# Performance work log

Hardware: AMD Instinct MI355X
Metric: run time of the kernel (lower is better)

## Reference

```python
import jax, jax.numpy as jnp
import numpy as np

NUM_BREAKPOINTS = 100  # module default
IMG_SHAPE = (1, 1, 4096, 8192)  # B must be 1: PWL(num_channels=1) sees (C*H*W, B)


def setup_inputs() -> dict:
    key = jax.random.key(0)
    k1, k2, k3, k4 = jax.random.split(key, 4)
    x = jax.random.uniform(k1, IMG_SHAPE, dtype=jnp.float32)
    # torchpwl.PWL parameters (num_channels=1): breakpoint x-positions, per-segment
    # slopes, and bias (function value at the leftmost breakpoint).
    x_positions = jax.random.uniform(k2, (1, NUM_BREAKPOINTS), dtype=jnp.float32)
    slopes = 1.0 + 0.1 * jax.random.normal(k3, (1, NUM_BREAKPOINTS), dtype=jnp.float32)
    biases = 0.05 * jax.random.normal(k4, (1,), dtype=jnp.float32)
    return {"x": x, "x_positions": x_positions, "slopes": slopes, "biases": biases}


def _pwl(x_flat, x_positions, slopes, biases):
    # Sloped piecewise-linear function (torchpwl.BaseSlopedPWL math), 1 channel.
    # x_flat: (N,), x_positions/slopes: (1, K), biases: (1,)
    K = x_positions.shape[1]
    sorted_x = jnp.sort(x_positions, axis=1)                     # (1, K)
    skips = jnp.roll(sorted_x, -1, axis=1) - sorted_x            # last entry never used
    cumsums = jnp.cumsum(skips * slopes, axis=1)[:, :-1]         # (1, K-1)
    betas = jnp.concatenate([biases[:, None], biases[:, None] + cumsums], axis=1)  # (1, K)
    # segment index: (# breakpoints <= x) clamped to [1, K], minus 1
    idx = jnp.clip(jnp.searchsorted(sorted_x[0], x_flat, side="right"), 1, K) - 1
    return betas[0, idx] + (x_flat - sorted_x[0, idx]) * slopes[0, idx]


def reference(x, x_positions, slopes, biases):
    # forward: flatten -> PWL -> clip(0,1) -> reshape (original returns [out])
    y = _pwl(x.reshape(-1), x_positions, slopes, biases)
    return jnp.clip(y, 0.0, 1.0).reshape(x.shape)
```

## Files before the change

### kernel.cpp

```cpp
#include <hip/hip_runtime.h>

#define K   100
#define NB  1024
#define BS  512
#define NBLK 1024

typedef float fvec4 __attribute__((ext_vector_type(4)));

__device__ __forceinline__ float pwl_eval(float xv,
                                          const float2* __restrict__ s_bab,
                                          const float* __restrict__ s_x,
                                          const float2* __restrict__ s_ab) {
  int b = (int)(xv * (float)NB);
  b = min(max(b, 0), NB - 1);
  float2 ab = s_bab[b];
  if (__float_as_uint(ab.x) == 0x7f800000u) {
    unsigned p = __float_as_uint(ab.y);
    int lo = (int)(p & 0xffffu);
    int hi = (int)(p >> 16);
    while (lo < hi) {
      int mid = (lo + hi) >> 1;
      if (s_x[mid] <= xv) lo = mid + 1; else hi = mid;
    }
    int idx = min(max(lo, 1), K) - 1;
    ab = s_ab[idx];
  }
  float y = fmaf(xv, ab.x, ab.y);
  return fminf(fmaxf(y, 0.0f), 1.0f);
}

__global__ __launch_bounds__(BS) void pwl_fused_kernel(
    const fvec4* __restrict__ x, const float* __restrict__ xp,
    const float* __restrict__ sl, const float* __restrict__ bias,
    fvec4* __restrict__ out, int n4, int n) {
  __shared__ float s_pos[K];
  __shared__ float s_slope[K];
  __shared__ float s_x[K];
  __shared__ float s_c[K];
  __shared__ float2 s_ab[K];
  __shared__ unsigned short s_cnt[NB + 1];
  __shared__ float2 s_bab[NB];

  const int t = threadIdx.x;

  if (t < K) { s_pos[t] = xp[t]; s_slope[t] = sl[t]; }
  __syncthreads();

  if (t < K) {
    float v = s_pos[t];
    int r = 0;
    for (int j = 0; j < K; ++j) {
      float u = s_pos[j];
      r += ((u < v) || (u == v && j < t)) ? 1 : 0;
    }
    s_x[r] = v;
  }
  __syncthreads();

  if (t < K - 1) s_c[t] = (s_x[t + 1] - s_x[t]) * s_slope[t];
  __syncthreads();
  for (int off = 1; off < K - 1; off <<= 1) {
    float v = 0.0f;
    if (t >= off && t < K - 1) v = s_c[t - off];
    __syncthreads();
    if (t < K - 1) s_c[t] += v;
    __syncthreads();
  }
  if (t < K) {
    float beta = bias[0] + (t ? s_c[t - 1] : 0.0f);
    float a = s_slope[t];
    s_ab[t] = make_float2(a, beta - s_x[t] * a);
  }
  __syncthreads();

  for (int e = t; e <= NB; e += BS) {
    float ev = (float)e * (1.0f / (float)NB);
    int lo = 0, hi = K;
    while (lo < hi) {
      int mid = (lo + hi) >> 1;
      if (s_x[mid] <= ev) lo = mid + 1; else hi = mid;
    }
    s_cnt[e] = (unsigned short)lo;
  }
  __syncthreads();

  for (int b = t; b < NB; b += BS) {
    int lo = s_cnt[b], hi = s_cnt[b + 1];
    float2 e;
    if (lo == hi) {
      int idx = min(max(lo, 1), K) - 1;
      e = s_ab[idx];
    } else {
      e.x = __builtin_huge_valf();
      e.y = __uint_as_float((unsigned)lo | ((unsigned)hi << 16));
    }
    s_bab[b] = e;
  }
  __syncthreads();

  const int stride = NBLK * BS;
  int i = blockIdx.x * BS + t;
  if (i < n4) {
    fvec4 v = __builtin_nontemporal_load(&x[i]);
    while (true) {
      int inext = i + stride;
      bool more = inext < n4;
      fvec4 vn = {};
      if (more) vn = __builtin_nontemporal_load(&x[inext]);
      fvec4 r;
      r.x = pwl_eval(v.x, s_bab, s_x, s_ab);
      r.y = pwl_eval(v.y, s_bab, s_x, s_ab);
      r.z = pwl_eval(v.z, s_bab, s_x, s_ab);
      r.w = pwl_eval(v.w, s_bab, s_x, s_ab);
      __builtin_nontemporal_store(r, &out[i]);
      if (!more) break;
      v = vn;
      i = inext;
    }
  }

  if (blockIdx.x == 0) {
    const float* xs = (const float*)x;
    float* os = (float*)out;
    for (int j = (n4 << 2) + t; j < n; j += BS) {
      os[j] = pwl_eval(xs[j], s_bab, s_x, s_ab);
    }
  }
}

extern "C" void kernel_launch(void* const* d_in, const int* in_sizes, int n_in,
                              void* d_out, int out_size, void* d_ws, size_t ws_size,
                              hipStream_t stream) {
  const float* x    = (const float*)d_in[0];
  const float* xp   = (const float*)d_in[1];
  const float* sl   = (const float*)d_in[2];
  const float* bias = (const float*)d_in[3];
  float* out = (float*)d_out;

  const int n  = in_sizes[0];
  const int n4 = n >> 2;

  pwl_fused_kernel<<<NBLK, BS, 0, stream>>>(
      (const fvec4*)x, xp, sl, bias, (fvec4*)out, n4, n);
}
```

Measured before the change: 247.4 us.

## Split table construction into a single-block setup kernel feeding main kernel

Moves the per-block sort, prefix sum and bucket-table construction into a separate one-block setup kernel that writes the tables to workspace. The main kernel then only copies those tables into shared memory. It also splits the bucket table into separate a/b float arrays, switches to 2048 blocks of 256 threads, and drops nontemporal loads. This removes redundant setup work in every block at the cost of an extra kernel launch and a serial dependency between the two kernels.

```diff
diff --git a/kernel.cpp b/kernel.cpp
--- a/kernel.cpp
+++ b/kernel.cpp
@@ -1,46 +1,22 @@
 #include <hip/hip_runtime.h>
 
-#define K   100
-#define NB  1024
-#define BS  512
-#define NBLK 1024
+#define K  100
+#define NB 1024
 
 typedef float fvec4 __attribute__((ext_vector_type(4)));
 
-__device__ __forceinline__ float pwl_eval(float xv,
-                                          const float2* __restrict__ s_bab,
-                                          const float* __restrict__ s_x,
-                                          const float2* __restrict__ s_ab) {
-  int b = (int)(xv * (float)NB);
-  b = min(max(b, 0), NB - 1);
-  float2 ab = s_bab[b];
-  if (__float_as_uint(ab.x) == 0x7f800000u) {
-    unsigned p = __float_as_uint(ab.y);
-    int lo = (int)(p & 0xffffu);
-    int hi = (int)(p >> 16);
-    while (lo < hi) {
-      int mid = (lo + hi) >> 1;
-      if (s_x[mid] <= xv) lo = mid + 1; else hi = mid;
-    }
-    int idx = min(max(lo, 1), K) - 1;
-    ab = s_ab[idx];
-  }
-  float y = fmaf(xv, ab.x, ab.y);
-  return fminf(fmaxf(y, 0.0f), 1.0f);
-}
-
-__global__ __launch_bounds__(BS) void pwl_fused_kernel(
-    const fvec4* __restrict__ x, const float* __restrict__ xp,
-    const float* __restrict__ sl, const float* __restrict__ bias,
-    fvec4* __restrict__ out, int n4, int n) {
+__global__ __launch_bounds__(1024) void pwl_setup_kernel(
+    const float* __restrict__ xp, const float* __restrict__ sl,
+    const float* __restrict__ bias, float* __restrict__ a_g,
+    float* __restrict__ b_g, float* __restrict__ sx_g,
+    float2* __restrict__ ab_g) {
   __shared__ float s_pos[K];
   __shared__ float s_slope[K];
   __shared__ float s_x[K];
   __shared__ float s_c[K];
-  __shared__ float2 s_ab[K];
+  __shared__ float s_sa[K];
+  __shared__ float s_sb[K];
   __shared__ unsigned short s_cnt[NB + 1];
-  __shared__ float2 s_bab[NB];
-
   const int t = threadIdx.x;
 
   if (t < K) { s_pos[t] = xp[t]; s_slope[t] = sl[t]; }
@@ -69,11 +45,17 @@
   if (t < K) {
     float beta = bias[0] + (t ? s_c[t - 1] : 0.0f);
     float a = s_slope[t];
-    s_ab[t] = make_float2(a, beta - s_x[t] * a);
+    s_sa[t] = a;
+    s_sb[t] = beta - s_x[t] * a;
   }
   __syncthreads();
 
-  for (int e = t; e <= NB; e += BS) {
+  if (t < K) {
+    sx_g[t] = s_x[t];
+    ab_g[t] = make_float2(s_sa[t], s_sb[t]);
+  }
+
+  for (int e = t; e <= NB; e += blockDim.x) {
     float ev = (float)e * (1.0f / (float)NB);
     int lo = 0, hi = K;
     while (lo < hi) {
@@ -84,34 +66,80 @@
   }
   __syncthreads();
 
-  for (int b = t; b < NB; b += BS) {
+  for (int b = t; b < NB; b += blockDim.x) {
     int lo = s_cnt[b], hi = s_cnt[b + 1];
-    float2 e;
+    float av, bv;
     if (lo == hi) {
       int idx = min(max(lo, 1), K) - 1;
-      e = s_ab[idx];
+      av = s_sa[idx];
+      bv = s_sb[idx];
     } else {
-      e.x = __builtin_huge_valf();
-      e.y = __uint_as_float((unsigned)lo | ((unsigned)hi << 16));
+      av = __builtin_huge_valf();
+      bv = __uint_as_float((unsigned)lo | ((unsigned)hi << 16));
     }
-    s_bab[b] = e;
+    a_g[b] = av;
+    b_g[b] = bv;
+  }
+}
+
+__device__ __forceinline__ float pwl_eval(float xv,
+                                          const float* __restrict__ s_a,
+                                          const float* __restrict__ s_b,
+                                          const float* __restrict__ s_x,
+                                          const float2* __restrict__ s_ab) {
+  int bkt = (int)(xv * (float)NB);
+  bkt = min(max(bkt, 0), NB - 1);
+  float a = s_a[bkt];
+  float b = s_b[bkt];
+  if (__float_as_uint(a) == 0x7f800000u) {
+    unsigned p = __float_as_uint(b);
+    int lo = (int)(p & 0xffffu);
+    int hi = (int)(p >> 16);
+    while (lo < hi) {
+      int mid = (lo + hi) >> 1;
+      if (s_x[mid] <= xv) lo = mid + 1; else hi = mid;
+    }
+    int idx = min(max(lo, 1), K) - 1;
+    float2 ab = s_ab[idx];
+    a = ab.x;
+    b = ab.y;
+  }
+  float y = fmaf(xv, a, b);
+  return fminf(fmaxf(y, 0.0f), 1.0f);
+}
+
+__global__ __launch_bounds__(256) void pwl_main_kernel(
+    const fvec4* __restrict__ x, const float* __restrict__ a_g,
+    const float* __restrict__ b_g, const float* __restrict__ sx_g,
+    const float2* __restrict__ ab_g, fvec4* __restrict__ out, int n4, int n) {
+  __shared__ float s_a[NB];
+  __shared__ float s_b[NB];
+  __shared__ float s_x[K];
+  __shared__ float2 s_ab[K];
+  for (int i = threadIdx.x; i < NB; i += blockDim.x) {
+    s_a[i] = a_g[i];
+    s_b[i] = b_g[i];
+  }
+  if (threadIdx.x < K) {
+    s_x[threadIdx.x] = sx_g[threadIdx.x];
+    s_ab[threadIdx.x] = ab_g[threadIdx.x];
   }
   __syncthreads();
 
-  const int stride = NBLK * BS;
-  int i = blockIdx.x * BS + t;
+  const int stride = gridDim.x * blockDim.x;
+  int i = blockIdx.x * blockDim.x + threadIdx.x;
   if (i < n4) {
-    fvec4 v = __builtin_nontemporal_load(&x[i]);
+    fvec4 v = x[i];
     while (true) {
       int inext = i + stride;
       bool more = inext < n4;
       fvec4 vn = {};
-      if (more) vn = __builtin_nontemporal_load(&x[inext]);
+      if (more) vn = x[inext];
       fvec4 r;
-      r.x = pwl_eval(v.x, s_bab, s_x, s_ab);
-      r.y = pwl_eval(v.y, s_bab, s_x, s_ab);
-      r.z = pwl_eval(v.z, s_bab, s_x, s_ab);
-      r.w = pwl_eval(v.w, s_bab, s_x, s_ab);
+      r.x = pwl_eval(v.x, s_a, s_b, s_x, s_ab);
+      r.y = pwl_eval(v.y, s_a, s_b, s_x, s_ab);
+      r.z = pwl_eval(v.z, s_a, s_b, s_x, s_ab);
+      r.w = pwl_eval(v.w, s_a, s_b, s_x, s_ab);
       __builtin_nontemporal_store(r, &out[i]);
       if (!more) break;
       v = vn;
@@ -122,8 +150,8 @@
   if (blockIdx.x == 0) {
     const float* xs = (const float*)x;
     float* os = (float*)out;
-    for (int j = (n4 << 2) + t; j < n; j += BS) {
-      os[j] = pwl_eval(xs[j], s_bab, s_x, s_ab);
+    for (int j = (n4 << 2) + threadIdx.x; j < n; j += blockDim.x) {
+      os[j] = pwl_eval(xs[j], s_a, s_b, s_x, s_ab);
     }
   }
 }
@@ -137,9 +165,18 @@
   const float* bias = (const float*)d_in[3];
   float* out = (float*)d_out;
 
+  float* a_tab = (float*)d_ws;
+  float* b_tab = (float*)((char*)d_ws + NB * 4);
+  float* sx    = (float*)((char*)d_ws + NB * 8);
+  float2* ab   = (float2*)((char*)d_ws + NB * 8 + 512);
+
   const int n  = in_sizes[0];
   const int n4 = n >> 2;
 
-  pwl_fused_kernel<<<NBLK, BS, 0, stream>>>(
-      (const fvec4*)x, xp, sl, bias, (fvec4*)out, n4, n);
+  pwl_setup_kernel<<<1, 1024, 0, stream>>>(xp, sl, bias, a_tab, b_tab, sx, ab);
+
+  const int threads = 256;
+  const int blocks  = 2048;
+  pwl_main_kernel<<<blocks, threads, 0, stream>>>(
+      (const fvec4*)x, a_tab, b_tab, sx, ab, (fvec4*)out, n4, n);
 }
```

Result: no change. 243.0 us (-1.8%).
